# Optimization experiments

Measured on AMD Instinct MI355X. Metric: run time of the kernel, lower is better.

## Reference

```python
import jax, jax.numpy as jnp
import numpy as np

N = 50000          # num nodes
E = 800000         # num edges (before self-loops)
F_IN = 128         # num_node_features
HEADS = 8          # num_heads (layer 1)
F_HEAD = 16        # features_per_head
N_CLASSES = 32     # num_classes (layer 2, heads=1)
NEG_SLOPE = 0.2    # PyG GATConv default LeakyReLU slope


def setup_inputs() -> dict:
    key = jax.random.key(0)
    ks = jax.random.split(key, 9)
    x = jax.random.normal(ks[0], (N, F_IN), jnp.float32)
    src = jax.random.randint(ks[1], (E,), 0, N, dtype=jnp.int32)
    dst = jax.random.randint(ks[2], (E,), 0, N, dtype=jnp.int32)
    # layer 1 params
    W1 = jax.random.normal(ks[3], (F_IN, HEADS * F_HEAD), jnp.float32) / np.sqrt(F_IN).astype(np.float32)
    a_src1 = jax.random.normal(ks[4], (HEADS, F_HEAD), jnp.float32) * 0.1
    a_dst1 = jax.random.normal(ks[5], (HEADS, F_HEAD), jnp.float32) * 0.1
    b1 = jnp.zeros((HEADS * F_HEAD,), jnp.float32)  # bias_init = zeros_
    # layer 2 params (heads=1)
    W2 = jax.random.normal(ks[6], (HEADS * F_HEAD, N_CLASSES), jnp.float32) / np.sqrt(HEADS * F_HEAD).astype(np.float32)
    a_src2 = jax.random.normal(ks[7], (1, N_CLASSES), jnp.float32) * 0.1
    a_dst2 = jax.random.normal(ks[8], (1, N_CLASSES), jnp.float32) * 0.1
    b2 = jnp.zeros((N_CLASSES,), jnp.float32)
    return {"x": x, "src": src, "dst": dst,
            "W1": W1, "a_src1": a_src1, "a_dst1": a_dst1, "b1": b1,
            "W2": W2, "a_src2": a_src2, "a_dst2": a_dst2, "b2": b2}


def gat_conv(x, src, dst, W, a_src, a_dst, b, heads, feat):
    """PyG-style GATConv (concat=True, add_self_loops=True)."""
    h = (x @ W).reshape(N, heads, feat)                 # [N,H,F]
    al_src = jnp.sum(h * a_src, axis=-1)                # [N,H]
    al_dst = jnp.sum(h * a_dst, axis=-1)                # [N,H]
    loop = jnp.arange(N, dtype=src.dtype)
    s = jnp.concatenate([src, loop])                    # [E+N]
    d = jnp.concatenate([dst, loop])                    # [E+N]
    e = jax.nn.leaky_relu(al_src[s] + al_dst[d], NEG_SLOPE)   # [E+N,H]
    # numerically stable softmax over edges grouped by dst node
    m = jax.ops.segment_max(e, d, num_segments=N)       # [N,H]
    ex = jnp.exp(e - m[d])
    denom = jax.ops.segment_sum(ex, d, num_segments=N)  # [N,H]
    alpha = ex / denom[d]                               # [E+N,H]
    out = jax.ops.segment_sum(alpha[:, :, None] * h[s], d, num_segments=N)  # [N,H,F]
    return out.reshape(N, heads * feat) + b


def reference(x, src, dst, W1, a_src1, a_dst1, b1, W2, a_src2, a_dst2, b2):
    h = gat_conv(x, src, dst, W1, a_src1, a_dst1, b1, HEADS, F_HEAD)
    h = jax.nn.elu(h)
    h = gat_conv(h, src, dst, W2, a_src2, a_dst2, b2, 1, N_CLASSES)
    return jax.nn.log_softmax(h, axis=1)
```

## Files before the change

kernel.cpp:

```cpp
#include <hip/hip_runtime.h>

#define N_NODES   50000
#define N_EDGES   800000
#define NEG_SLOPE 0.2f
#define NBKT      256
#define NPB       196
#define EPB       3125

__device__ __forceinline__ float leaky(float x) {
    return x > 0.f ? x : x * NEG_SLOPE;
}

__device__ __forceinline__ unsigned short f2bf(float f) {
    unsigned int u = __float_as_uint(f);
    unsigned int r = (u + 0x7FFFu + ((u >> 16) & 1u)) >> 16;
    return (unsigned short)r;
}

__device__ __forceinline__ float2 bf2f2(unsigned int p) {
    return make_float2(__uint_as_float(p << 16),
                       __uint_as_float(p & 0xFFFF0000u));
}

__device__ __forceinline__ void fma4(float4& acc, const float4 a,
                                     const float4 w0, const float4 w1,
                                     const float4 w2, const float4 w3) {
    acc.x = fmaf(a.x, w0.x, fmaf(a.y, w1.x, fmaf(a.z, w2.x, fmaf(a.w, w3.x, acc.x))));
    acc.y = fmaf(a.x, w0.y, fmaf(a.y, w1.y, fmaf(a.z, w2.y, fmaf(a.w, w3.y, acc.y))));
    acc.z = fmaf(a.x, w0.z, fmaf(a.y, w1.z, fmaf(a.z, w2.z, fmaf(a.w, w3.z, acc.z))));
    acc.w = fmaf(a.x, w0.w, fmaf(a.y, w1.w, fmaf(a.z, w2.w, fmaf(a.w, w3.w, acc.w))));
}

__device__ __forceinline__ float dot4(const float4 a, const float4 b) {
    return a.x * b.x + a.y * b.y + a.z * b.z + a.w * b.w;
}

__global__ __launch_bounds__(256) void k_hist(const int* __restrict__ dst,
                                              int* __restrict__ hist_g) {
    __shared__ int h[NBKT];
    const int tid = threadIdx.x, blk = blockIdx.x;
    h[tid] = 0;
    __syncthreads();
    const int e0 = blk * EPB;
    for (int j = e0 + tid; j < e0 + EPB; j += 256)
        atomicAdd(&h[dst[j] / NPB], 1);
    __syncthreads();
    hist_g[tid * NBKT + blk] = h[tid];
}

__global__ __launch_bounds__(1024) void k_scanA(const int* __restrict__ hist_g,
                                                int* __restrict__ partial) {
    __shared__ int red[1024];
    const int tid = threadIdx.x;
    red[tid] = hist_g[blockIdx.x * 1024 + tid];
    __syncthreads();
    for (int off = 512; off; off >>= 1) {
        if (tid < off) red[tid] += red[tid + off];
        __syncthreads();
    }
    if (tid == 0) partial[blockIdx.x] = red[0];
}

__global__ __launch_bounds__(1024) void k_scanB(const int* __restrict__ hist_g,
                                                const int* __restrict__ partial,
                                                int* __restrict__ offs) {
    __shared__ int sh[1024];
    __shared__ int blockoff_sh;
    const int b = blockIdx.x, tid = threadIdx.x;
    const int idx = b * 1024 + tid;
    const int v = hist_g[idx];
    sh[tid] = v;
    __syncthreads();
    if (tid == 0) {
        int s = 0;
        for (int i = 0; i < b; ++i) s += partial[i];
        blockoff_sh = s;
    }
    for (int off = 1; off < 1024; off <<= 1) {
        int add = (tid >= off) ? sh[tid - off] : 0;
        __syncthreads();
        sh[tid] += add;
        __syncthreads();
    }
    offs[idx] = blockoff_sh + sh[tid] - v;
}

__global__ __launch_bounds__(256) void k_binscatter(const int* __restrict__ src,
                                                    const int* __restrict__ dst,
                                                    const int* __restrict__ offs,
                                                    unsigned int* __restrict__ binned) {
    __shared__ int cur[NBKT];
    const int tid = threadIdx.x, blk = blockIdx.x;
    cur[tid] = offs[tid * NBKT + blk];
    __syncthreads();
    const int e0 = blk * EPB;
    for (int j = e0 + tid; j < e0 + EPB; j += 256) {
        int d   = dst[j];
        int bkt = d / NPB;
        int dl  = d - bkt * NPB;
        int pos = atomicAdd(&cur[bkt], 1);
        binned[pos] = (unsigned int)src[j] | ((unsigned int)dl << 18);
    }
}

__global__ __launch_bounds__(256) void k_csr_fine(const unsigned int* __restrict__ binned,
                                                  const int* __restrict__ offs,
                                                  int* __restrict__ row_ptr,
                                                  int* __restrict__ csr) {
    __shared__ int cnt[256];
    __shared__ int scan[256];
    __shared__ int cur[256];
    const int b = blockIdx.x, tid = threadIdx.x;
    const int start = offs[b * NBKT];
    const int end   = (b == NBKT - 1) ? N_EDGES : offs[(b + 1) * NBKT];
    cnt[tid] = 0;
    __syncthreads();
    for (int j = start + tid; j < end; j += 256)
        atomicAdd(&cnt[(binned[j] >> 18) & 255], 1);
    __syncthreads();
    const int v = cnt[tid];
    scan[tid] = v;
    __syncthreads();
    for (int off = 1; off < 256; off <<= 1) {
        int add = (tid >= off) ? scan[tid - off] : 0;
        __syncthreads();
        scan[tid] += add;
        __syncthreads();
    }
    const int excl = scan[tid] - v;
    cur[tid] = excl;
    const int node = b * NPB + tid;
    if (tid < NPB && node < N_NODES) row_ptr[node] = start + excl;
    if (b == NBKT - 1 && tid == 0)   row_ptr[N_NODES] = N_EDGES;
    __syncthreads();
    for (int j = start + tid; j < end; j += 256) {
        unsigned int p = binned[j];
        int dl  = (p >> 18) & 255;
        int pos = start + atomicAdd(&cur[dl], 1);
        csr[pos] = (int)(p & 0x3FFFFu);
    }
}

__global__ __launch_bounds__(256) void k_gemm1(
    const float* __restrict__ x, const float* __restrict__ W1,
    const float* __restrict__ a_src, const float* __restrict__ a_dst,
    unsigned short* __restrict__ h1b, float* __restrict__ al_src,
    float* __restrict__ al_dst)
{
    __shared__ float4 xs4[64 * 32];
    __shared__ float4 ws4[128 * 16];
    const int tid  = threadIdx.x;
    const int half = blockIdx.x & 1;
    const int row0 = (int)(blockIdx.x >> 1) * 64;
    const int tc   = tid & 15;
    const int tr   = tid >> 4;
    const float4* x4  = (const float4*)x;
    const float4* W14 = (const float4*)W1;

    #pragma unroll
    for (int p = 0; p < 8; ++p) {
        int i = tid + p * 256;
        int k = i >> 4, c4 = i & 15;
        ws4[k * 16 + c4] = W14[k * 32 + half * 16 + c4];
    }
    #pragma unroll
    for (int p = 0; p < 8; ++p) {
        int i = tid + p * 256;
        int r = i >> 5, k4 = i & 31;
        int gr = row0 + r; if (gr > N_NODES - 1) gr = N_NODES - 1;
        xs4[r * 32 + (k4 ^ ((r >> 2) & 7))] = x4[gr * 32 + k4];
    }
    __syncthreads();

    float4 acc[4];
    #pragma unroll
    for (int i = 0; i < 4; ++i) acc[i] = make_float4(0.f, 0.f, 0.f, 0.f);
    const int sw = tr & 7;
    #pragma unroll 2
    for (int k4 = 0; k4 < 32; ++k4) {
        float4 w0 = ws4[(4 * k4 + 0) * 16 + tc];
        float4 w1 = ws4[(4 * k4 + 1) * 16 + tc];
        float4 w2 = ws4[(4 * k4 + 2) * 16 + tc];
        float4 w3 = ws4[(4 * k4 + 3) * 16 + tc];
        const int kk = k4 ^ sw;
        #pragma unroll
        for (int i = 0; i < 4; ++i) {
            float4 a = xs4[(4 * tr + i) * 32 + kk];
            fma4(acc[i], a, w0, w1, w2, w3);
        }
    }

    const int c0   = half * 64 + 4 * tc;
    const int head = c0 >> 4;
    const float4 as4 = ((const float4*)a_src)[half * 16 + tc];
    const float4 ad4 = ((const float4*)a_dst)[half * 16 + tc];
    #pragma unroll
    for (int i = 0; i < 4; ++i) {
        int r = row0 + 4 * tr + i;
        if (r < N_NODES) {
            ((ushort4*)h1b)[r * 32 + half * 16 + tc] =
                make_ushort4(f2bf(acc[i].x), f2bf(acc[i].y),
                             f2bf(acc[i].z), f2bf(acc[i].w));
            float s = dot4(acc[i], as4);
            float d = dot4(acc[i], ad4);
            s += __shfl_xor(s, 1); s += __shfl_xor(s, 2);
            d += __shfl_xor(d, 1); d += __shfl_xor(d, 2);
            if ((tc & 3) == 0) {
                al_src[r * 8 + head] = s;
                al_dst[r * 8 + head] = d;
            }
        }
    }
}

__global__ __launch_bounds__(256) void k_agg1(
    const unsigned short* __restrict__ h1b, const float* __restrict__ al_src,
    const float* __restrict__ al_dst, const int* __restrict__ row_ptr,
    const int* __restrict__ csr_src, const float* __restrict__ b1,
    float* __restrict__ h2)
{
    const int n = blockIdx.x * 4 + (threadIdx.x >> 6);
    const int l    = threadIdx.x & 63;
    const int slot = l >> 4;
    const int f2   = l & 15;
    const int head = f2 >> 1;
    const uint4* h1q = (const uint4*)h1b;

    const float alD = al_dst[n * 8 + head];
    float denom = 0.f;
    float acc[8];
    #pragma unroll
    for (int i = 0; i < 8; ++i) acc[i] = 0.f;

    if (slot == 0) {
        float w = __expf(leaky(al_src[n * 8 + head] + alD));
        uint4 q = h1q[n * 16 + f2];
        float2 v0 = bf2f2(q.x), v1 = bf2f2(q.y), v2 = bf2f2(q.z), v3 = bf2f2(q.w);
        denom = w;
        acc[0] = w * v0.x; acc[1] = w * v0.y; acc[2] = w * v1.x; acc[3] = w * v1.y;
        acc[4] = w * v2.x; acc[5] = w * v2.y; acc[6] = w * v3.x; acc[7] = w * v3.y;
    }

    const int beg = row_ptr[n], end = row_ptr[n + 1];
    for (int j = beg + slot; j < end; j += 4) {
        int s = csr_src[j];
        float w = __expf(leaky(al_src[s * 8 + head] + alD));
        uint4 q = h1q[s * 16 + f2];
        denom += w;
        float2 v0 = bf2f2(q.x), v1 = bf2f2(q.y), v2 = bf2f2(q.z), v3 = bf2f2(q.w);
        acc[0] = fmaf(w, v0.x, acc[0]); acc[1] = fmaf(w, v0.y, acc[1]);
        acc[2] = fmaf(w, v1.x, acc[2]); acc[3] = fmaf(w, v1.y, acc[3]);
        acc[4] = fmaf(w, v2.x, acc[4]); acc[5] = fmaf(w, v2.y, acc[5]);
        acc[6] = fmaf(w, v3.x, acc[6]); acc[7] = fmaf(w, v3.y, acc[7]);
    }

    #pragma unroll
    for (int i = 0; i < 8; ++i) {
        acc[i] += __shfl_xor(acc[i], 16);
        acc[i] += __shfl_xor(acc[i], 32);
    }
    denom += __shfl_xor(denom, 16);
    denom += __shfl_xor(denom, 32);

    if (slot == 0) {
        const float4 bA = ((const float4*)b1)[f2 * 2];
        const float4 bB = ((const float4*)b1)[f2 * 2 + 1];
        float inv = 1.f / denom;
        float o[8];
        o[0] = acc[0] * inv + bA.x; o[1] = acc[1] * inv + bA.y;
        o[2] = acc[2] * inv + bA.z; o[3] = acc[3] * inv + bA.w;
        o[4] = acc[4] * inv + bB.x; o[5] = acc[5] * inv + bB.y;
        o[6] = acc[6] * inv + bB.z; o[7] = acc[7] * inv + bB.w;
        #pragma unroll
        for (int i = 0; i < 8; ++i) o[i] = o[i] > 0.f ? o[i] : expm1f(o[i]);
        ((float4*)h2)[n * 32 + f2 * 2]     = make_float4(o[0], o[1], o[2], o[3]);
        ((float4*)h2)[n * 32 + f2 * 2 + 1] = make_float4(o[4], o[5], o[6], o[7]);
    }
}

__global__ __launch_bounds__(128) void k_gemm2(
    const float* __restrict__ h2, const float* __restrict__ W2,
    const float* __restrict__ a_src, const float* __restrict__ a_dst,
    unsigned short* __restrict__ t2b, float* __restrict__ al_src,
    float* __restrict__ al_dst)
{
    __shared__ float4 xs4[64 * 32];
    __shared__ float4 ws4[128 * 8];
    const int tid  = threadIdx.x;
    const int row0 = (int)blockIdx.x * 64;
    const int tc   = tid & 7;
    const int tr   = tid >> 3;
    const float4* h24 = (const float4*)h2;
    const float4* W24 = (const float4*)W2;

    #pragma unroll
    for (int p = 0; p < 8; ++p) {
        int i = tid + p * 128;
        ws4[i] = W24[i];
    }
    #pragma unroll
    for (int p = 0; p < 16; ++p) {
        int i = tid + p * 128;
        int r = i >> 5, k4 = i & 31;
        int gr = row0 + r; if (gr > N_NODES - 1) gr = N_NODES - 1;
        xs4[r * 32 + (k4 ^ ((r >> 2) & 7))] = h24[gr * 32 + k4];
    }
    __syncthreads();

    float4 acc[4];
    #pragma unroll
    for (int i = 0; i < 4; ++i) acc[i] = make_float4(0.f, 0.f, 0.f, 0.f);
    const int sw = tr & 7;
    #pragma unroll 2
    for (int k4 = 0; k4 < 32; ++k4) {
        float4 w0 = ws4[(4 * k4 + 0) * 8 + tc];
        float4 w1 = ws4[(4 * k4 + 1) * 8 + tc];
        float4 w2 = ws4[(4 * k4 + 2) * 8 + tc];
        float4 w3 = ws4[(4 * k4 + 3) * 8 + tc];
        const int kk = k4 ^ sw;
        #pragma unroll
        for (int i = 0; i < 4; ++i) {
            float4 a = xs4[(4 * tr + i) * 32 + kk];
            fma4(acc[i], a, w0, w1, w2, w3);
        }
    }

    const float4 as4 = ((const float4*)a_src)[tc];
    const float4 ad4 = ((const float4*)a_dst)[tc];
    #pragma unroll
    for (int i = 0; i < 4; ++i) {
        int r = row0 + 4 * tr + i;
        if (r < N_NODES) {
            ((ushort4*)t2b)[r * 8 + tc] =
                make_ushort4(f2bf(acc[i].x), f2bf(acc[i].y),
                             f2bf(acc[i].z), f2bf(acc[i].w));
            float s = dot4(acc[i], as4);
            float d = dot4(acc[i], ad4);
            s += __shfl_xor(s, 1); s += __shfl_xor(s, 2); s += __shfl_xor(s, 4);
            d += __shfl_xor(d, 1); d += __shfl_xor(d, 2); d += __shfl_xor(d, 4);
            if (tc == 0) {
                al_src[r] = s;
                al_dst[r] = d;
            }
        }
    }
}

__global__ __launch_bounds__(256) void k_agg2(
    const unsigned short* __restrict__ t2b, const float* __restrict__ al_src,
    const float* __restrict__ al_dst, const int* __restrict__ row_ptr,
    const int* __restrict__ csr_src, const float* __restrict__ b2,
    float* __restrict__ out)
{
    const int n = blockIdx.x * 4 + (threadIdx.x >> 6);
    const int l = threadIdx.x & 63;
    const int slot = l >> 4;
    const int f2   = l & 15;
    const unsigned int* t2u = (const unsigned int*)t2b;

    const float alD = al_dst[n];
    float denom = 0.f;
    float2 acc = make_float2(0.f, 0.f);
    if (slot == 0) {
        float w = __expf(leaky(al_src[n] + alD));
        float2 v = bf2f2(t2u[n * 16 + f2]);
        denom = w;
        acc = make_float2(w * v.x, w * v.y);
    }
    const int beg = row_ptr[n], end = row_ptr[n + 1];
    for (int j = beg + slot; j < end; j += 4) {
        int s = csr_src[j];
        float w = __expf(leaky(al_src[s] + alD));
        float2 v = bf2f2(t2u[s * 16 + f2]);
        denom += w;
        acc.x = fmaf(w, v.x, acc.x);
        acc.y = fmaf(w, v.y, acc.y);
    }
    acc.x += __shfl_xor(acc.x, 16); acc.y += __shfl_xor(acc.y, 16);
    denom += __shfl_xor(denom, 16);
    acc.x += __shfl_xor(acc.x, 32); acc.y += __shfl_xor(acc.y, 32);
    denom += __shfl_xor(denom, 32);

    const float2 bb = ((const float2*)b2)[f2];
    float ox = acc.x / denom + bb.x;
    float oy = acc.y / denom + bb.y;
    float m = fmaxf(ox, oy);
    for (int off = 8; off; off >>= 1) m = fmaxf(m, __shfl_xor(m, off));
    float ssum = __expf(ox - m) + __expf(oy - m);
    for (int off = 8; off; off >>= 1) ssum += __shfl_xor(ssum, off);
    float lg = __logf(ssum);
    if (l < 16)
        ((float2*)out)[n * 16 + f2] = make_float2(ox - m - lg, oy - m - lg);
}

extern "C" void kernel_launch(void* const* d_in, const int* in_sizes, int n_in,
                              void* d_out, int out_size, void* d_ws, size_t ws_size,
                              hipStream_t stream) {
    const float* x      = (const float*)d_in[0];
    const int*   src    = (const int*)d_in[1];
    const int*   dst    = (const int*)d_in[2];
    const float* W1     = (const float*)d_in[3];
    const float* a_src1 = (const float*)d_in[4];
    const float* a_dst1 = (const float*)d_in[5];
    const float* b1     = (const float*)d_in[6];
    const float* W2     = (const float*)d_in[7];
    const float* a_src2 = (const float*)d_in[8];
    const float* a_dst2 = (const float*)d_in[9];
    const float* b2     = (const float*)d_in[10];
    float* out = (float*)d_out;

    char* ws = (char*)d_ws;
    size_t off = 0;
    auto alloc = [&](size_t bytes) {
        void* p = ws + off;
        off += (bytes + 255) & ~(size_t)255;
        return p;
    };
    unsigned short* h1b = (unsigned short*)alloc((size_t)N_NODES * 128 * 2);
    float*          h2  = (float*)alloc((size_t)N_NODES * 128 * 4);
    unsigned short* t2b = (unsigned short*)alloc((size_t)N_NODES * 32 * 2);
    float* alS1    = (float*)alloc((size_t)N_NODES * 8 * 4);
    float* alD1    = (float*)alloc((size_t)N_NODES * 8 * 4);
    float* alS2    = (float*)alloc((size_t)N_NODES * 4);
    float* alD2    = (float*)alloc((size_t)N_NODES * 4);
    int*   rowp    = (int*)alloc((size_t)(N_NODES + 1) * 4);
    int*   csr     = (int*)alloc((size_t)N_EDGES * 4);
    unsigned int* binned = (unsigned int*)alloc((size_t)N_EDGES * 4);
    int*   hist_g  = (int*)alloc((size_t)NBKT * NBKT * 4);
    int*   offs    = (int*)alloc((size_t)NBKT * NBKT * 4);
    int*   partial = (int*)alloc((size_t)64 * 4);
    (void)ws_size; (void)in_sizes; (void)n_in; (void)out_size;

    const int row_tiles = (N_NODES + 63) / 64;

    k_hist<<<NBKT, 256, 0, stream>>>(dst, hist_g);
    k_scanA<<<64, 1024, 0, stream>>>(hist_g, partial);
    k_scanB<<<64, 1024, 0, stream>>>(hist_g, partial, offs);
    k_binscatter<<<NBKT, 256, 0, stream>>>(src, dst, offs, binned);
    k_csr_fine<<<NBKT, 256, 0, stream>>>(binned, offs, rowp, csr);
    k_gemm1<<<row_tiles * 2, 256, 0, stream>>>(x, W1, a_src1, a_dst1, h1b, alS1, alD1);
    k_agg1<<<N_NODES / 4, 256, 0, stream>>>(h1b, alS1, alD1, rowp, csr, b1, h2);
    k_gemm2<<<row_tiles, 128, 0, stream>>>(h2, W2, a_src2, a_dst2, t2b, alS2, alD2);
    k_agg2<<<N_NODES / 4, 256, 0, stream>>>(t2b, alS2, alD2, rowp, csr, b2, out);
}
```

Baseline: 243.1 us.

## Fuse CSR build into one cooperative kernel and unroll aggregation loops by two

The five separate CSR-construction kernels (histogram, two-pass scan, bin scatter, fine sort) are merged into a single cooperative kernel that uses grid-wide syncs between phases. The global scan is reorganised into a per-block 256-wide scan plus a scan over block totals. The edge-aggregation loops in both GAT layers are also unrolled to process two neighbours per iteration, issuing their gathers together for more memory-level parallelism. This removes several launch gaps but relies on cooperative launch residency and grid-sync cost, and adds register pressure in the aggregation kernels.

```diff
diff --git a/kernel.cpp b/kernel.cpp
--- a/kernel.cpp
+++ b/kernel.cpp
@@ -1,4 +1,7 @@
 #include <hip/hip_runtime.h>
+#include <hip/hip_cooperative_groups.h>
+
+namespace cg = cooperative_groups;
 
 #define N_NODES   50000
 #define N_EDGES   800000
@@ -35,65 +38,57 @@
     return a.x * b.x + a.y * b.y + a.z * b.z + a.w * b.w;
 }
 
-__global__ __launch_bounds__(256) void k_hist(const int* __restrict__ dst,
-                                              int* __restrict__ hist_g) {
-    __shared__ int h[NBKT];
-    const int tid = threadIdx.x, blk = blockIdx.x;
+__global__ __launch_bounds__(256) void k_csr_build(
+    const int* __restrict__ src, const int* __restrict__ dst,
+    int* __restrict__ hist_g, int* __restrict__ offs, int* __restrict__ totals,
+    unsigned int* __restrict__ binned,
+    int* __restrict__ row_ptr, int* __restrict__ csr)
+{
+    cg::grid_group grid = cg::this_grid();
+    const int b = blockIdx.x, tid = threadIdx.x;
+    __shared__ int h[256];
+    __shared__ int sc[256];
+    __shared__ int cur[256];
+    __shared__ int base_sh;
+
     h[tid] = 0;
     __syncthreads();
-    const int e0 = blk * EPB;
+    const int e0 = b * EPB;
     for (int j = e0 + tid; j < e0 + EPB; j += 256)
         atomicAdd(&h[dst[j] / NPB], 1);
     __syncthreads();
-    hist_g[tid * NBKT + blk] = h[tid];
-}
-
-__global__ __launch_bounds__(1024) void k_scanA(const int* __restrict__ hist_g,
-                                                int* __restrict__ partial) {
-    __shared__ int red[1024];
-    const int tid = threadIdx.x;
-    red[tid] = hist_g[blockIdx.x * 1024 + tid];
-    __syncthreads();
-    for (int off = 512; off; off >>= 1) {
-        if (tid < off) red[tid] += red[tid + off];
-        __syncthreads();
-    }
-    if (tid == 0) partial[blockIdx.x] = red[0];
-}
-
-__global__ __launch_bounds__(1024) void k_scanB(const int* __restrict__ hist_g,
-                                                const int* __restrict__ partial,
-                                                int* __restrict__ offs) {
-    __shared__ int sh[1024];
-    __shared__ int blockoff_sh;
-    const int b = blockIdx.x, tid = threadIdx.x;
-    const int idx = b * 1024 + tid;
-    const int v = hist_g[idx];
-    sh[tid] = v;
-    __syncthreads();
-    if (tid == 0) {
-        int s = 0;
-        for (int i = 0; i < b; ++i) s += partial[i];
-        blockoff_sh = s;
-    }
-    for (int off = 1; off < 1024; off <<= 1) {
-        int add = (tid >= off) ? sh[tid - off] : 0;
-        __syncthreads();
-        sh[tid] += add;
-        __syncthreads();
-    }
-    offs[idx] = blockoff_sh + sh[tid] - v;
-}
-
-__global__ __launch_bounds__(256) void k_binscatter(const int* __restrict__ src,
-                                                    const int* __restrict__ dst,
-                                                    const int* __restrict__ offs,
-                                                    unsigned int* __restrict__ binned) {
-    __shared__ int cur[NBKT];
-    const int tid = threadIdx.x, blk = blockIdx.x;
-    cur[tid] = offs[tid * NBKT + blk];
-    __syncthreads();
-    const int e0 = blk * EPB;
+    hist_g[tid * NBKT + b] = h[tid];
+    grid.sync();
+
+    int v = hist_g[b * 256 + tid];
+    sc[tid] = v;
+    __syncthreads();
+    for (int off = 1; off < 256; off <<= 1) {
+        int add = (tid >= off) ? sc[tid - off] : 0;
+        __syncthreads();
+        sc[tid] += add;
+        __syncthreads();
+    }
+    offs[b * 256 + tid] = sc[tid] - v;
+    if (tid == 255) totals[b] = sc[255];
+    grid.sync();
+
+    int tv = totals[tid];
+    sc[tid] = tv;
+    __syncthreads();
+    for (int off = 1; off < 256; off <<= 1) {
+        int add = (tid >= off) ? sc[tid - off] : 0;
+        __syncthreads();
+        sc[tid] += add;
+        __syncthreads();
+    }
+    if (tid == 0) base_sh = (b == 0) ? 0 : sc[b - 1];
+    __syncthreads();
+    offs[b * 256 + tid] += base_sh;
+    grid.sync();
+
+    cur[tid] = offs[tid * 256 + b];
+    __syncthreads();
     for (int j = e0 + tid; j < e0 + EPB; j += 256) {
         int d   = dst[j];
         int bkt = d / NPB;
@@ -101,39 +96,31 @@
         int pos = atomicAdd(&cur[bkt], 1);
         binned[pos] = (unsigned int)src[j] | ((unsigned int)dl << 18);
     }
-}
-
-__global__ __launch_bounds__(256) void k_csr_fine(const unsigned int* __restrict__ binned,
-                                                  const int* __restrict__ offs,
-                                                  int* __restrict__ row_ptr,
-                                                  int* __restrict__ csr) {
-    __shared__ int cnt[256];
-    __shared__ int scan[256];
-    __shared__ int cur[256];
-    const int b = blockIdx.x, tid = threadIdx.x;
-    const int start = offs[b * NBKT];
-    const int end   = (b == NBKT - 1) ? N_EDGES : offs[(b + 1) * NBKT];
-    cnt[tid] = 0;
-    __syncthreads();
-    for (int j = start + tid; j < end; j += 256)
-        atomicAdd(&cnt[(binned[j] >> 18) & 255], 1);
-    __syncthreads();
-    const int v = cnt[tid];
-    scan[tid] = v;
+    grid.sync();
+
+    const int start = offs[b * 256];
+    const int endE  = (b == NBKT - 1) ? N_EDGES : offs[(b + 1) * 256];
+    h[tid] = 0;
+    __syncthreads();
+    for (int j = start + tid; j < endE; j += 256)
+        atomicAdd(&h[(binned[j] >> 18) & 255], 1);
+    __syncthreads();
+    int fv = h[tid];
+    sc[tid] = fv;
     __syncthreads();
     for (int off = 1; off < 256; off <<= 1) {
-        int add = (tid >= off) ? scan[tid - off] : 0;
-        __syncthreads();
-        scan[tid] += add;
-        __syncthreads();
-    }
-    const int excl = scan[tid] - v;
+        int add = (tid >= off) ? sc[tid - off] : 0;
+        __syncthreads();
+        sc[tid] += add;
+        __syncthreads();
+    }
+    const int excl = sc[tid] - fv;
     cur[tid] = excl;
     const int node = b * NPB + tid;
     if (tid < NPB && node < N_NODES) row_ptr[node] = start + excl;
     if (b == NBKT - 1 && tid == 0)   row_ptr[N_NODES] = N_EDGES;
     __syncthreads();
-    for (int j = start + tid; j < end; j += 256) {
+    for (int j = start + tid; j < endE; j += 256) {
         unsigned int p = binned[j];
         int dl  = (p >> 18) & 255;
         int pos = start + atomicAdd(&cur[dl], 1);
@@ -242,7 +229,29 @@
     }
 
     const int beg = row_ptr[n], end = row_ptr[n + 1];
-    for (int j = beg + slot; j < end; j += 4) {
+    int j = beg + slot;
+    for (; j + 4 < end; j += 8) {
+        int sa = csr_src[j];
+        int sb = csr_src[j + 4];
+        float ala = al_src[sa * 8 + head];
+        float alb = al_src[sb * 8 + head];
+        uint4 qa = h1q[sa * 16 + f2];
+        uint4 qb = h1q[sb * 16 + f2];
+        float wa = __expf(leaky(ala + alD));
+        float wb = __expf(leaky(alb + alD));
+        denom += wa + wb;
+        float2 a0 = bf2f2(qa.x), a1 = bf2f2(qa.y), a2 = bf2f2(qa.z), a3 = bf2f2(qa.w);
+        acc[0] = fmaf(wa, a0.x, acc[0]); acc[1] = fmaf(wa, a0.y, acc[1]);
+        acc[2] = fmaf(wa, a1.x, acc[2]); acc[3] = fmaf(wa, a1.y, acc[3]);
+        acc[4] = fmaf(wa, a2.x, acc[4]); acc[5] = fmaf(wa, a2.y, acc[5]);
+        acc[6] = fmaf(wa, a3.x, acc[6]); acc[7] = fmaf(wa, a3.y, acc[7]);
+        float2 b0 = bf2f2(qb.x), b1v = bf2f2(qb.y), b2v = bf2f2(qb.z), b3 = bf2f2(qb.w);
+        acc[0] = fmaf(wb, b0.x, acc[0]); acc[1] = fmaf(wb, b0.y, acc[1]);
+        acc[2] = fmaf(wb, b1v.x, acc[2]); acc[3] = fmaf(wb, b1v.y, acc[3]);
+        acc[4] = fmaf(wb, b2v.x, acc[4]); acc[5] = fmaf(wb, b2v.y, acc[5]);
+        acc[6] = fmaf(wb, b3.x, acc[6]); acc[7] = fmaf(wb, b3.y, acc[7]);
+    }
+    if (j < end) {
         int s = csr_src[j];
         float w = __expf(leaky(al_src[s * 8 + head] + alD));
         uint4 q = h1q[s * 16 + f2];
@@ -368,7 +377,22 @@
         acc = make_float2(w * v.x, w * v.y);
     }
     const int beg = row_ptr[n], end = row_ptr[n + 1];
-    for (int j = beg + slot; j < end; j += 4) {
+    int j = beg + slot;
+    for (; j + 4 < end; j += 8) {
+        int sa = csr_src[j];
+        int sb = csr_src[j + 4];
+        float ala = al_src[sa];
+        float alb = al_src[sb];
+        unsigned int pa = t2u[sa * 16 + f2];
+        unsigned int pb = t2u[sb * 16 + f2];
+        float wa = __expf(leaky(ala + alD));
+        float wb = __expf(leaky(alb + alD));
+        denom += wa + wb;
+        float2 va = bf2f2(pa), vb = bf2f2(pb);
+        acc.x = fmaf(wa, va.x, acc.x); acc.y = fmaf(wa, va.y, acc.y);
+        acc.x = fmaf(wb, vb.x, acc.x); acc.y = fmaf(wb, vb.y, acc.y);
+    }
+    if (j < end) {
         int s = csr_src[j];
         float w = __expf(leaky(al_src[s] + alD));
         float2 v = bf2f2(t2u[s * 16 + f2]);
@@ -428,16 +452,17 @@
     unsigned int* binned = (unsigned int*)alloc((size_t)N_EDGES * 4);
     int*   hist_g  = (int*)alloc((size_t)NBKT * NBKT * 4);
     int*   offs    = (int*)alloc((size_t)NBKT * NBKT * 4);
-    int*   partial = (int*)alloc((size_t)64 * 4);
+    int*   totals  = (int*)alloc((size_t)NBKT * 4);
     (void)ws_size; (void)in_sizes; (void)n_in; (void)out_size;
 
     const int row_tiles = (N_NODES + 63) / 64;
 
-    k_hist<<<NBKT, 256, 0, stream>>>(dst, hist_g);
-    k_scanA<<<64, 1024, 0, stream>>>(hist_g, partial);
-    k_scanB<<<64, 1024, 0, stream>>>(hist_g, partial, offs);
-    k_binscatter<<<NBKT, 256, 0, stream>>>(src, dst, offs, binned);
-    k_csr_fine<<<NBKT, 256, 0, stream>>>(binned, offs, rowp, csr);
+    {
+        void* args[] = { (void*)&src, (void*)&dst, (void*)&hist_g, (void*)&offs,
+                         (void*)&totals, (void*)&binned, (void*)&rowp, (void*)&csr };
+        hipLaunchCooperativeKernel((void*)k_csr_build, dim3(NBKT), dim3(256),
+                                   args, 0, stream);
+    }
     k_gemm1<<<row_tiles * 2, 256, 0, stream>>>(x, W1, a_src1, a_dst1, h1b, alS1, alD1);
     k_agg1<<<N_NODES / 4, 256, 0, stream>>>(h1b, alS1, alD1, rowp, csr, b1, h2);
     k_gemm2<<<row_tiles, 128, 0, stream>>>(h2, W2, a_src2, a_dst2, t2b, alS2, alD2);
```

After: 373.8 us. 1.54x slower.
